# Optimization experiments

Hardware: AMD Instinct MI355X
Metric: run time of the kernel (lower is better)

Reference implementation:

```python
import jax, jax.numpy as jnp
import numpy as np

B, P, D = 64, 256, 768
S = P + 1            # class token + patches
GRID = 16.0          # sqrt(no_of_patches)
N_IMGS = 10000


def setup_inputs() -> dict:
    key = jax.random.key(0)
    ks = jax.random.split(key, 10)
    sc = 1.0 / np.sqrt(D)
    return {
        "x": jax.random.normal(ks[0], (B, S, D), jnp.float32),
        "img_ids": jax.random.randint(ks[1], (B,), 0, N_IMGS),
        "mask": jnp.ones((B, S), jnp.int32),
        "avgs": 0.1 * jax.random.normal(ks[2], (N_IMGS, 2, P), jnp.float32),
        "std_devs": jnp.ones((N_IMGS, 2, P), jnp.float32),
        "Wq": sc * jax.random.normal(ks[3], (D, D), jnp.float32),
        "bq": jnp.zeros((D,), jnp.float32),
        "Wk": sc * jax.random.normal(ks[4], (D, D), jnp.float32),
        "bk": jnp.zeros((D,), jnp.float32),
        "Wv": sc * jax.random.normal(ks[5], (D, D), jnp.float32),
        "bv": jnp.zeros((D,), jnp.float32),
        "noise_x": jax.random.normal(ks[6], (B, P), jnp.float32),  # torch.normal(0, sigma)
        "noise_y": jax.random.normal(ks[7], (B, P), jnp.float32),
    }


def reference(x, img_ids, mask, avgs, std_devs, Wq, bq, Wk, bk, Wv, bv, noise_x, noise_y):
    # nn.Linear: y = x @ W^T + b
    q = jnp.einsum("bsd,ed->bse", x, Wq) + bq  # (B,S,D)
    k = jnp.einsum("bsd,ed->bse", x, Wk) + bk
    v = jnp.einsum("bsd,ed->bse", x, Wv) + bv

    a = avgs[img_ids]       # (B,2,P)
    sd = std_devs[img_ids]  # (B,2,P)
    half = (GRID - 1.0) / 2.0
    kx = half * (1.0 + jnp.tanh((noise_x + a[:, 0]) * sd[:, 0]))  # (B,P) in (0, GRID-1)
    ky = half * (1.0 + jnp.tanh((noise_y + a[:, 1]) * sd[:, 1]))
    kx1, kx2 = jnp.ceil(kx), jnp.floor(kx)
    ky1, ky2 = jnp.ceil(ky), jnp.floor(ky)

    # corner order matches original: (x1,y1), (x2,y1), (x1,y2), (x2,y2)
    cx = jnp.stack([kx1, kx2, kx1, kx2], axis=1)  # (B,4,P)
    cy = jnp.stack([ky1, ky1, ky2, ky2], axis=1)
    idxs = jax.lax.stop_gradient(GRID * cy + cx).astype(jnp.int32)  # (B,4,P), < P

    sk = jnp.take_along_axis(k[:, None], idxs[..., None], axis=2)  # (B,4,P,D)
    sv = jnp.take_along_axis(v[:, None], idxs[..., None], axis=2)
    cls = jnp.ones((B, 4, 1, D), sk.dtype)
    skf = jnp.concatenate([cls, sk], axis=2)  # (B,4,S,D)
    svf = jnp.concatenate([cls, sv], axis=2)

    # score per query s against its 4 sampled corner keys; softmax over the 4 corners
    scores = jnp.einsum("bnsd,bsd->bsn", skf, q)   # (B,S,4)
    attn = jax.nn.softmax(scores, axis=-1)          # (B,S,4)
    attn_v = attn.transpose(0, 2, 1)[..., None] * svf  # (B,4,S,D)

    # bilinear weights (1-|cx-kx|)*(1-|cy-ky|); class-token weight fixed to 1
    w = (1.0 - jnp.abs(cx - kx[:, None])) * (1.0 - jnp.abs(cy - ky[:, None]))  # (B,4,P)
    wf = jnp.concatenate([jnp.ones((B, 4, 1), w.dtype), w], axis=2)  # (B,4,S)
    out = jnp.einsum("bns,bnsd->bsd", wf, attn_v)  # (B,S,D)
    return out
```

## Files before the change

### kernel.cpp

```cpp
#include <hip/hip_runtime.h>
#include <math.h>


typedef _Float16 f16x8 __attribute__((ext_vector_type(8)));
typedef _Float16 f16x4 __attribute__((ext_vector_type(4)));
typedef float    f32x4 __attribute__((ext_vector_type(4)));

#define MTOT 16448
#define DD   768
#define NC   2304
#define NT   12
#define XU   (129*12*1024)
#define WU   (18*12*1024)

__global__ __launch_bounds__(256) void prepass(
    const float* __restrict__ x,
    const float* __restrict__ Wq, const float* __restrict__ Wk, const float* __restrict__ Wv,
    _Float16* __restrict__ xp, _Float16* __restrict__ wp)
{
    const int gidx = blockIdx.x * 256 + threadIdx.x;
    const float* src;
    _Float16* dst;
    if (gidx < XU) {
        const int u = gidx & 1023, k = (gidx >> 10) % NT, tile = gidx / (NT * 1024);
        const int lane = u & 63, ksub = (u >> 6) & 1, mblk = u >> 7;
        int row = tile * 128 + mblk * 16 + (lane & 15);
        row = row < MTOT ? row : MTOT - 1;
        const int col = k * 64 + ksub * 32 + (lane >> 4) * 8;
        src = x + (size_t)row * DD + col;
        dst = xp + (size_t)gidx * 8;
    } else {
        const int g = gidx - XU;
        const int u = g & 1023, k = (g >> 10) % NT, tile = g / (NT * 1024);
        const int lane = u & 63, ksub = (u >> 6) & 1, mblk = u >> 7;
        const int wrow = tile * 128 + mblk * 16 + (lane & 15);
        const float* W = wrow < 768 ? Wq : (wrow < 1536 ? Wk : Wv);
        const int srow = wrow - (wrow < 768 ? 0 : (wrow < 1536 ? 768 : 1536));
        const int col = k * 64 + ksub * 32 + (lane >> 4) * 8;
        src = W + (size_t)srow * DD + col;
        dst = wp + (size_t)g * 8;
    }
    const float4 a = *(const float4*)src;
    const float4 b = *(const float4*)(src + 4);
    f16x8 o;
    o[0] = (_Float16)a.x; o[1] = (_Float16)a.y; o[2] = (_Float16)a.z; o[3] = (_Float16)a.w;
    o[4] = (_Float16)b.x; o[5] = (_Float16)b.y; o[6] = (_Float16)b.z; o[7] = (_Float16)b.w;
    *(f16x8*)dst = o;
}

__global__ __launch_bounds__(256) void qkv_gemm(
    const _Float16* __restrict__ xp, const _Float16* __restrict__ wp,
    const float* __restrict__ bq, const float* __restrict__ bk, const float* __restrict__ bv,
    _Float16* __restrict__ qkv)
{
    __shared__ __align__(16) _Float16 Ax[2][8192];
    __shared__ __align__(16) _Float16 Bx[2][8192];

    const int bid = blockIdx.x;
    const int xcd = bid & 7, pos = bid >> 3;
    const int q8 = 2322 / 8, r8 = 2322 % 8;
    const int orig = (xcd < r8) ? xcd * (q8 + 1) + pos
                                : r8 * (q8 + 1) + (xcd - r8) * q8 + pos;
    const int tileM = orig / 18, tileN = orig % 18;

    const int tid = threadIdx.x, lane = tid & 63, wid = tid >> 6;
    const int wm = wid >> 1, wn = wid & 1;
    const int r16 = lane & 15, kq = lane >> 4;

    const _Float16* Asrc = xp + (size_t)tileM * NT * 8192;
    const _Float16* Bsrc = wp + (size_t)tileN * NT * 8192;

    const f32x4 zero = {0.f, 0.f, 0.f, 0.f};
    f32x4 acc[4][4];
    #pragma unroll
    for (int i = 0; i < 4; ++i)
        #pragma unroll
        for (int j = 0; j < 4; ++j) acc[i][j] = zero;

    #pragma unroll
    for (int g = 0; g < 4; ++g) {
        const int u = g * 256 + tid;
        __builtin_amdgcn_global_load_lds(
            (const __attribute__((address_space(1))) void*)(Asrc + (size_t)u * 8),
            (__attribute__((address_space(3))) void*)(&Ax[0][u * 8]), 16, 0, 0);
        __builtin_amdgcn_global_load_lds(
            (const __attribute__((address_space(1))) void*)(Bsrc + (size_t)u * 8),
            (__attribute__((address_space(3))) void*)(&Bx[0][u * 8]), 16, 0, 0);
    }

    for (int t = 0; t < NT; ++t) {
        const int cur = t & 1;
        if (t + 1 < NT) {
            const size_t off = (size_t)(t + 1) * 8192;
            #pragma unroll
            for (int g = 0; g < 4; ++g) {
                const int u = g * 256 + tid;
                __builtin_amdgcn_global_load_lds(
                    (const __attribute__((address_space(1))) void*)(Asrc + off + (size_t)u * 8),
                    (__attribute__((address_space(3))) void*)(&Ax[cur ^ 1][u * 8]), 16, 0, 0);
                __builtin_amdgcn_global_load_lds(
                    (const __attribute__((address_space(1))) void*)(Bsrc + off + (size_t)u * 8),
                    (__attribute__((address_space(3))) void*)(&Bx[cur ^ 1][u * 8]), 16, 0, 0);
            }
            asm volatile("s_waitcnt vmcnt(8)" ::: "memory");
        } else {
            asm volatile("s_waitcnt vmcnt(0)" ::: "memory");
        }
        __builtin_amdgcn_s_barrier();
        __builtin_amdgcn_sched_barrier(0);

        #pragma unroll
        for (int s = 0; s < 2; ++s) {
            f16x8 a[4], b[4];
            #pragma unroll
            for (int i = 0; i < 4; ++i)
                a[i] = *(const f16x8*)(&Ax[cur][(((wm * 4 + i) * 2 + s) * 64 + lane) * 8]);
            #pragma unroll
            for (int j = 0; j < 4; ++j)
                b[j] = *(const f16x8*)(&Bx[cur][(((wn * 4 + j) * 2 + s) * 64 + lane) * 8]);
            #pragma unroll
            for (int i = 0; i < 4; ++i)
                #pragma unroll
                for (int j = 0; j < 4; ++j)
                    acc[i][j] = __builtin_amdgcn_mfma_f32_16x16x32_f16(a[i], b[j], acc[i][j], 0, 0, 0);
        }
        asm volatile("s_waitcnt lgkmcnt(0)" ::: "memory");
        __builtin_amdgcn_sched_barrier(0);
        __builtin_amdgcn_s_barrier();
        __builtin_amdgcn_sched_barrier(0);
    }

    const int sec = tileN / 6;
    const float* bias = sec == 0 ? bq : (sec == 1 ? bk : bv);
    const int bcol0 = (tileN % 6) * 128 + wn * 64;
    #pragma unroll
    for (int i = 0; i < 4; ++i) {
        const int row0 = tileM * 128 + wm * 64 + i * 16 + kq * 4;
        #pragma unroll
        for (int j = 0; j < 4; ++j) {
            const int col = tileN * 128 + wn * 64 + j * 16 + r16;
            const float bb = bias[bcol0 + j * 16 + r16];
            #pragma unroll
            for (int t = 0; t < 4; ++t) {
                const int row = row0 + t;
                if (row < MTOT)
                    qkv[(size_t)row * NC + col] = (_Float16)(acc[i][j][t] + bb);
            }
        }
    }
}

__global__ __launch_bounds__(256) void attn_gather(
    const _Float16* __restrict__ qkv,
    const int*   __restrict__ ids,
    const float* __restrict__ avgs,
    const float* __restrict__ stds,
    const float* __restrict__ nx,
    const float* __restrict__ ny,
    float* __restrict__ out)
{
    const int tid  = threadIdx.x;
    const int lane = tid & 63;
    const int bid = blockIdx.x;
    const int swz = (bid & 7) * 514 + (bid >> 3);
    const int gid = swz * 4 + (tid >> 6);
    const int b = gid / 257, s = gid % 257;
    float* orow = out + (size_t)gid * DD;

    if (s == 0) {
        const float4 one = make_float4(1.f, 1.f, 1.f, 1.f);
        #pragma unroll
        for (int j = 0; j < 3; ++j)
            *(float4*)(orow + 4 * lane + 256 * j) = one;
        return;
    }
    const int p   = s - 1;
    const int img = ids[b];
    const size_t ab = (size_t)img * 512 + p;
    const float a0 = avgs[ab], a1 = avgs[ab + 256];
    const float s0 = stds[ab], s1 = stds[ab + 256];
    const float kx = 7.5f * (1.f + tanhf((nx[b * 256 + p] + a0) * s0));
    const float ky = 7.5f * (1.f + tanhf((ny[b * 256 + p] + a1) * s1));
    const float kx1 = ceilf(kx), kx2 = floorf(kx);
    const float ky1 = ceilf(ky), ky2 = floorf(ky);
    const float cx[4] = {kx1, kx2, kx1, kx2};
    const float cy[4] = {ky1, ky1, ky2, ky2};
    int   idx[4];
    float w[4];
    #pragma unroll
    for (int n = 0; n < 4; ++n) {
        idx[n] = (int)(16.f * cy[n] + cx[n]);
        w[n]   = (1.f - fabsf(cx[n] - kx)) * (1.f - fabsf(cy[n] - ky));
    }

    const _Float16* qrow = qkv + (size_t)gid * NC;
    float qf[12];
    #pragma unroll
    for (int j = 0; j < 3; ++j) {
        const f16x4 v = *(const f16x4*)(qrow + lane * 4 + j * 256);
        qf[4 * j + 0] = (float)v[0]; qf[4 * j + 1] = (float)v[1];
        qf[4 * j + 2] = (float)v[2]; qf[4 * j + 3] = (float)v[3];
    }

    float sc[4];
    #pragma unroll
    for (int n = 0; n < 4; ++n) {
        const _Float16* krow = qkv + (size_t)(b * 257 + idx[n]) * NC + 768;
        float a = 0.f;
        #pragma unroll
        for (int j = 0; j < 3; ++j) {
            const f16x4 kv = *(const f16x4*)(krow + lane * 4 + j * 256);
            a += qf[4 * j + 0] * (float)kv[0] + qf[4 * j + 1] * (float)kv[1]
               + qf[4 * j + 2] * (float)kv[2] + qf[4 * j + 3] * (float)kv[3];
        }
        sc[n] = a;
    }
    #pragma unroll
    for (int n = 0; n < 4; ++n)
        for (int off = 32; off > 0; off >>= 1)
            sc[n] += __shfl_xor(sc[n], off);

    const float mx = fmaxf(fmaxf(sc[0], sc[1]), fmaxf(sc[2], sc[3]));
    const float e0 = expf(sc[0] - mx), e1 = expf(sc[1] - mx),
                e2 = expf(sc[2] - mx), e3 = expf(sc[3] - mx);
    const float inv = 1.f / (e0 + e1 + e2 + e3);
    const float coef[4] = {e0 * inv * w[0], e1 * inv * w[1], e2 * inv * w[2], e3 * inv * w[3]};

    const _Float16* vr0 = qkv + (size_t)(b * 257 + idx[0]) * NC + 1536;
    const _Float16* vr1 = qkv + (size_t)(b * 257 + idx[1]) * NC + 1536;
    const _Float16* vr2 = qkv + (size_t)(b * 257 + idx[2]) * NC + 1536;
    const _Float16* vr3 = qkv + (size_t)(b * 257 + idx[3]) * NC + 1536;
    #pragma unroll
    for (int j = 0; j < 3; ++j) {
        const int d = lane * 4 + j * 256;
        const f16x4 v0 = *(const f16x4*)(vr0 + d);
        const f16x4 v1 = *(const f16x4*)(vr1 + d);
        const f16x4 v2 = *(const f16x4*)(vr2 + d);
        const f16x4 v3 = *(const f16x4*)(vr3 + d);
        float4 o;
        o.x = coef[0] * (float)v0[0] + coef[1] * (float)v1[0] + coef[2] * (float)v2[0] + coef[3] * (float)v3[0];
        o.y = coef[0] * (float)v0[1] + coef[1] * (float)v1[1] + coef[2] * (float)v2[1] + coef[3] * (float)v3[1];
        o.z = coef[0] * (float)v0[2] + coef[1] * (float)v1[2] + coef[2] * (float)v2[2] + coef[3] * (float)v3[2];
        o.w = coef[0] * (float)v0[3] + coef[1] * (float)v1[3] + coef[2] * (float)v2[3] + coef[3] * (float)v3[3];
        *(float4*)(orow + d) = o;
    }
}

extern "C" void kernel_launch(void* const* d_in, const int* in_sizes, int n_in,
                              void* d_out, int out_size, void* d_ws, size_t ws_size,
                              hipStream_t stream) {
    const float* x    = (const float*)d_in[0];
    const int*   ids  = (const int*)  d_in[1];
    const float* avgs = (const float*)d_in[3];
    const float* stds = (const float*)d_in[4];
    const float* Wq   = (const float*)d_in[5];
    const float* bq   = (const float*)d_in[6];
    const float* Wk   = (const float*)d_in[7];
    const float* bk   = (const float*)d_in[8];
    const float* Wv   = (const float*)d_in[9];
    const float* bv   = (const float*)d_in[10];
    const float* nx   = (const float*)d_in[11];
    const float* ny   = (const float*)d_in[12];
    float* out = (float*)d_out;

    char* ws = (char*)d_ws;
    _Float16* qkv = (_Float16*)ws;
    _Float16* xp  = (_Float16*)(ws + 75792384);
    _Float16* wp  = (_Float16*)(ws + 75792384 + 25362432);

    prepass<<<(XU + WU) / 256, 256, 0, stream>>>(x, Wq, Wk, Wv, xp, wp);
    qkv_gemm<<<2322, 256, 0, stream>>>(xp, wp, bq, bk, bv, qkv);
    attn_gather<<<4112, 256, 0, stream>>>(qkv, ids, avgs, stds, nx, ny, out);
}
```

Before: 133.3 us.

## Use 256x256 GEMM tiles with 512 threads and row-major fp16 prepass

```diff
diff --git a/kernel.cpp b/kernel.cpp
--- a/kernel.cpp
+++ b/kernel.cpp
@@ -9,36 +9,28 @@
 #define MTOT 16448
 #define DD   768
 #define NC   2304
-#define NT   12
-#define XU   (129*12*1024)
-#define WU   (18*12*1024)
+#define KT   12
+#define XE   (MTOT*DD/8)
+#define WE   (NC*DD/8)
 
 __global__ __launch_bounds__(256) void prepass(
     const float* __restrict__ x,
     const float* __restrict__ Wq, const float* __restrict__ Wk, const float* __restrict__ Wv,
-    _Float16* __restrict__ xp, _Float16* __restrict__ wp)
+    _Float16* __restrict__ xr, _Float16* __restrict__ wr)
 {
     const int gidx = blockIdx.x * 256 + threadIdx.x;
     const float* src;
     _Float16* dst;
-    if (gidx < XU) {
-        const int u = gidx & 1023, k = (gidx >> 10) % NT, tile = gidx / (NT * 1024);
-        const int lane = u & 63, ksub = (u >> 6) & 1, mblk = u >> 7;
-        int row = tile * 128 + mblk * 16 + (lane & 15);
-        row = row < MTOT ? row : MTOT - 1;
-        const int col = k * 64 + ksub * 32 + (lane >> 4) * 8;
-        src = x + (size_t)row * DD + col;
-        dst = xp + (size_t)gidx * 8;
+    if (gidx < XE) {
+        src = x + (size_t)gidx * 8;
+        dst = xr + (size_t)gidx * 8;
     } else {
-        const int g = gidx - XU;
-        const int u = g & 1023, k = (g >> 10) % NT, tile = g / (NT * 1024);
-        const int lane = u & 63, ksub = (u >> 6) & 1, mblk = u >> 7;
-        const int wrow = tile * 128 + mblk * 16 + (lane & 15);
+        const int g = gidx - XE;
+        const int wrow = g / 96, c8 = g % 96;
         const float* W = wrow < 768 ? Wq : (wrow < 1536 ? Wk : Wv);
         const int srow = wrow - (wrow < 768 ? 0 : (wrow < 1536 ? 768 : 1536));
-        const int col = k * 64 + ksub * 32 + (lane >> 4) * 8;
-        src = W + (size_t)srow * DD + col;
-        dst = wp + (size_t)g * 8;
+        src = W + (size_t)srow * DD + c8 * 8;
+        dst = wr + (size_t)g * 8;
     }
     const float4 a = *(const float4*)src;
     const float4 b = *(const float4*)(src + 4);
@@ -48,103 +40,155 @@
     *(f16x8*)dst = o;
 }
 
-__global__ __launch_bounds__(256) void qkv_gemm(
-    const _Float16* __restrict__ xp, const _Float16* __restrict__ wp,
+#define GLD(srcp, ldsp) \
+    __builtin_amdgcn_global_load_lds( \
+        (const __attribute__((address_space(1))) void*)(srcp), \
+        (__attribute__((address_space(3))) void*)(ldsp), 16, 0, 0)
+
+__global__ __launch_bounds__(512, 2) void qkv_gemm(
+    const _Float16* __restrict__ xr, const _Float16* __restrict__ wr,
     const float* __restrict__ bq, const float* __restrict__ bk, const float* __restrict__ bv,
     _Float16* __restrict__ qkv)
 {
-    __shared__ __align__(16) _Float16 Ax[2][8192];
-    __shared__ __align__(16) _Float16 Bx[2][8192];
+    __shared__ __align__(16) _Float16 Ax[2][16384];
+    __shared__ __align__(16) _Float16 Bx[2][16384];
 
     const int bid = blockIdx.x;
     const int xcd = bid & 7, pos = bid >> 3;
-    const int q8 = 2322 / 8, r8 = 2322 % 8;
-    const int orig = (xcd < r8) ? xcd * (q8 + 1) + pos
-                                : r8 * (q8 + 1) + (xcd - r8) * q8 + pos;
-    const int tileM = orig / 18, tileN = orig % 18;
+    const int orig = (xcd < 1) ? pos : 74 + (xcd - 1) * 73 + pos;
+    const int tileM = orig / 9, tileN = orig % 9;
 
     const int tid = threadIdx.x, lane = tid & 63, wid = tid >> 6;
-    const int wm = wid >> 1, wn = wid & 1;
+    const int wm = wid >> 2, wn = wid & 3;
     const int r16 = lane & 15, kq = lane >> 4;
 
-    const _Float16* Asrc = xp + (size_t)tileM * NT * 8192;
-    const _Float16* Bsrc = wp + (size_t)tileN * NT * 8192;
+    int offA[4], offB[4];
+    #pragma unroll
+    for (int g = 0; g < 4; ++g) {
+        const int mblk = g * 4 + (wid >> 1);
+        const int ks = wid & 1;
+        int ra = tileM * 256 + mblk * 16 + r16;
+        ra = ra < MTOT ? ra : MTOT - 1;
+        const int rb = tileN * 256 + mblk * 16 + r16;
+        offA[g] = ra * DD + ks * 32 + kq * 8;
+        offB[g] = rb * DD + ks * 32 + kq * 8;
+    }
 
     const f32x4 zero = {0.f, 0.f, 0.f, 0.f};
-    f32x4 acc[4][4];
-    #pragma unroll
-    for (int i = 0; i < 4; ++i)
+    f32x4 acc[8][4];
+    #pragma unroll
+    for (int i = 0; i < 8; ++i)
         #pragma unroll
         for (int j = 0; j < 4; ++j) acc[i][j] = zero;
 
     #pragma unroll
     for (int g = 0; g < 4; ++g) {
-        const int u = g * 256 + tid;
-        __builtin_amdgcn_global_load_lds(
-            (const __attribute__((address_space(1))) void*)(Asrc + (size_t)u * 8),
-            (__attribute__((address_space(3))) void*)(&Ax[0][u * 8]), 16, 0, 0);
-        __builtin_amdgcn_global_load_lds(
-            (const __attribute__((address_space(1))) void*)(Bsrc + (size_t)u * 8),
-            (__attribute__((address_space(3))) void*)(&Bx[0][u * 8]), 16, 0, 0);
-    }
-
-    for (int t = 0; t < NT; ++t) {
+        const int c0 = g * 512 + wid * 64;
+        GLD(xr + offA[g], &Ax[0][c0 * 8]);
+        GLD(wr + offB[g], &Bx[0][c0 * 8]);
+    }
+
+    for (int t = 0; t < KT; ++t) {
         const int cur = t & 1;
-        if (t + 1 < NT) {
-            const size_t off = (size_t)(t + 1) * 8192;
+        if (t + 1 < KT) {
+            const int ko = (t + 1) * 64;
             #pragma unroll
             for (int g = 0; g < 4; ++g) {
-                const int u = g * 256 + tid;
-                __builtin_amdgcn_global_load_lds(
-                    (const __attribute__((address_space(1))) void*)(Asrc + off + (size_t)u * 8),
-                    (__attribute__((address_space(3))) void*)(&Ax[cur ^ 1][u * 8]), 16, 0, 0);
-                __builtin_amdgcn_global_load_lds(
-                    (const __attribute__((address_space(1))) void*)(Bsrc + off + (size_t)u * 8),
-                    (__attribute__((address_space(3))) void*)(&Bx[cur ^ 1][u * 8]), 16, 0, 0);
+                const int c0 = g * 512 + wid * 64;
+                GLD(xr + offA[g] + ko, &Ax[cur ^ 1][c0 * 8]);
+                GLD(wr + offB[g] + ko, &Bx[cur ^ 1][c0 * 8]);
             }
             asm volatile("s_waitcnt vmcnt(8)" ::: "memory");
         } else {
             asm volatile("s_waitcnt vmcnt(0)" ::: "memory");
         }
+        __builtin_amdgcn_sched_barrier(0);
         __builtin_amdgcn_s_barrier();
         __builtin_amdgcn_sched_barrier(0);
 
-        #pragma unroll
-        for (int s = 0; s < 2; ++s) {
-            f16x8 a[4], b[4];
-            #pragma unroll
-            for (int i = 0; i < 4; ++i)
-                a[i] = *(const f16x8*)(&Ax[cur][(((wm * 4 + i) * 2 + s) * 64 + lane) * 8]);
-            #pragma unroll
-            for (int j = 0; j < 4; ++j)
-                b[j] = *(const f16x8*)(&Bx[cur][(((wn * 4 + j) * 2 + s) * 64 + lane) * 8]);
-            #pragma unroll
-            for (int i = 0; i < 4; ++i)
+        f16x8 bf[4][2], a0[4][2], a1[4][2];
+        #pragma unroll
+        for (int j = 0; j < 4; ++j)
+            #pragma unroll
+            for (int ks = 0; ks < 2; ++ks)
+                bf[j][ks] = *(const f16x8*)(&Bx[cur][(((wn * 4 + j) * 2 + ks) * 64 + lane) * 8]);
+        #pragma unroll
+        for (int i = 0; i < 4; ++i)
+            #pragma unroll
+            for (int ks = 0; ks < 2; ++ks)
+                a0[i][ks] = *(const f16x8*)(&Ax[cur][(((wm * 8 + i) * 2 + ks) * 64 + lane) * 8]);
+        asm volatile("s_waitcnt lgkmcnt(0)" ::: "memory");
+        __builtin_amdgcn_sched_barrier(0);
+
+        __builtin_amdgcn_s_setprio(1);
+        #pragma unroll
+        for (int i = 0; i < 4; ++i)
+            #pragma unroll
+            for (int j = 0; j < 2; ++j)
                 #pragma unroll
-                for (int j = 0; j < 4; ++j)
-                    acc[i][j] = __builtin_amdgcn_mfma_f32_16x16x32_f16(a[i], b[j], acc[i][j], 0, 0, 0);
-        }
+                for (int ks = 0; ks < 2; ++ks)
+                    acc[i][j] = __builtin_amdgcn_mfma_f32_16x16x32_f16(a0[i][ks], bf[j][ks], acc[i][j], 0, 0, 0);
+        __builtin_amdgcn_s_setprio(0);
+        __builtin_amdgcn_sched_barrier(0);
+
+        #pragma unroll
+        for (int i = 0; i < 4; ++i)
+            #pragma unroll
+            for (int ks = 0; ks < 2; ++ks)
+                a1[i][ks] = *(const f16x8*)(&Ax[cur][(((wm * 8 + 4 + i) * 2 + ks) * 64 + lane) * 8]);
+        __builtin_amdgcn_sched_barrier(0);
+
+        __builtin_amdgcn_s_setprio(1);
+        #pragma unroll
+        for (int i = 0; i < 4; ++i)
+            #pragma unroll
+            for (int j = 2; j < 4; ++j)
+                #pragma unroll
+                for (int ks = 0; ks < 2; ++ks)
+                    acc[i][j] = __builtin_amdgcn_mfma_f32_16x16x32_f16(a0[i][ks], bf[j][ks], acc[i][j], 0, 0, 0);
+        __builtin_amdgcn_s_setprio(0);
         asm volatile("s_waitcnt lgkmcnt(0)" ::: "memory");
         __builtin_amdgcn_sched_barrier(0);
+
+        __builtin_amdgcn_s_setprio(1);
+        #pragma unroll
+        for (int i = 0; i < 4; ++i)
+            #pragma unroll
+            for (int j = 0; j < 2; ++j)
+                #pragma unroll
+                for (int ks = 0; ks < 2; ++ks)
+                    acc[4 + i][j] = __builtin_amdgcn_mfma_f32_16x16x32_f16(a1[i][ks], bf[j][ks], acc[4 + i][j], 0, 0, 0);
+        __builtin_amdgcn_s_setprio(0);
+        __builtin_amdgcn_sched_barrier(0);
+
+        __builtin_amdgcn_s_setprio(1);
+        #pragma unroll
+        for (int i = 0; i < 4; ++i)
+            #pragma unroll
+            for (int j = 2; j < 4; ++j)
+                #pragma unroll
+                for (int ks = 0; ks < 2; ++ks)
+                    acc[4 + i][j] = __builtin_amdgcn_mfma_f32_16x16x32_f16(a1[i][ks], bf[j][ks], acc[4 + i][j], 0, 0, 0);
+        __builtin_amdgcn_s_setprio(0);
+        __builtin_amdgcn_sched_barrier(0);
         __builtin_amdgcn_s_barrier();
         __builtin_amdgcn_sched_barrier(0);
     }
 
-    const int sec = tileN / 6;
-    const float* bias = sec == 0 ? bq : (sec == 1 ? bk : bv);
-    const int bcol0 = (tileN % 6) * 128 + wn * 64;
-    #pragma unroll
-    for (int i = 0; i < 4; ++i) {
-        const int row0 = tileM * 128 + wm * 64 + i * 16 + kq * 4;
+    const float* bias = tileN < 3 ? bq : (tileN < 6 ? bk : bv);
+    const int bcolbase = (tileN % 3) * 256 + wn * 64;
+    #pragma unroll
+    for (int i = 0; i < 8; ++i) {
+        const int row0 = tileM * 256 + wm * 128 + i * 16 + kq * 4;
         #pragma unroll
         for (int j = 0; j < 4; ++j) {
-            const int col = tileN * 128 + wn * 64 + j * 16 + r16;
-            const float bb = bias[bcol0 + j * 16 + r16];
-            #pragma unroll
-            for (int t = 0; t < 4; ++t) {
-                const int row = row0 + t;
+            const int col = tileN * 256 + wn * 64 + j * 16 + r16;
+            const float bb = bias[bcolbase + j * 16 + r16];
+            #pragma unroll
+            for (int tt = 0; tt < 4; ++tt) {
+                const int row = row0 + tt;
                 if (row < MTOT)
-                    qkv[(size_t)row * NC + col] = (_Float16)(acc[i][j][t] + bb);
+                    qkv[(size_t)row * NC + col] = (_Float16)(acc[i][j][tt] + bb);
             }
         }
     }
@@ -265,10 +309,10 @@
 
     char* ws = (char*)d_ws;
     _Float16* qkv = (_Float16*)ws;
-    _Float16* xp  = (_Float16*)(ws + 75792384);
-    _Float16* wp  = (_Float16*)(ws + 75792384 + 25362432);
-
-    prepass<<<(XU + WU) / 256, 256, 0, stream>>>(x, Wq, Wk, Wv, xp, wp);
-    qkv_gemm<<<2322, 256, 0, stream>>>(xp, wp, bq, bk, bv, qkv);
+    _Float16* xr  = (_Float16*)(ws + 75792384);
+    _Float16* wr  = (_Float16*)(ws + 75792384 + 25264128);
+
+    prepass<<<(XE + WE) / 256, 256, 0, stream>>>(x, Wq, Wk, Wv, xr, wr);
+    qkv_gemm<<<585, 512, 0, stream>>>(xr, wr, bq, bk, bv, qkv);
     attn_gather<<<4112, 256, 0, stream>>>(qkv, ids, avgs, stds, nx, ny, out);
 }
```

Measured after the change: 184.8 us. +38.6%, slower.
